# Kernel tuning notes

Measured on AMD Instinct MI355X. Metric: run time of the kernel, lower is better.

## Reference

```python
import jax, jax.numpy as jnp
import numpy as np

NUM_LAYER = 5
NUM_FEATURES = 128
DIM = 256
NUM_BOND_TYPE = 6
NUM_BOND_DIR = 3
BN_EPS = 1e-5


def setup_inputs() -> dict:
    key = jax.random.key(0)
    ks = jax.random.split(key, 16)
    N, E = 100000, 400000
    x = jax.random.normal(ks[0], (N, NUM_FEATURES), dtype=jnp.float32)
    edge_index = jax.random.randint(ks[1], (2, E), 0, N, dtype=jnp.int32)
    edge_attr = jax.random.randint(ks[2], (E, 2), 0, 3, dtype=jnp.int32)
    s = 0.05
    Wl = jax.random.normal(ks[3], (NUM_FEATURES, DIM), dtype=jnp.float32) * s
    bl = jnp.zeros((DIM,), dtype=jnp.float32)
    W1 = jax.random.normal(ks[4], (NUM_LAYER, DIM, 2 * DIM), dtype=jnp.float32) * s
    b1 = jnp.zeros((NUM_LAYER, 2 * DIM), dtype=jnp.float32)
    W2 = jax.random.normal(ks[5], (NUM_LAYER, 2 * DIM, DIM), dtype=jnp.float32) * s
    b2 = jnp.zeros((NUM_LAYER, DIM), dtype=jnp.float32)
    E1 = jax.random.normal(ks[6], (NUM_LAYER, NUM_BOND_TYPE, DIM), dtype=jnp.float32) * s
    E2 = jax.random.normal(ks[7], (NUM_LAYER, NUM_BOND_DIR, DIM), dtype=jnp.float32) * s
    gamma = jnp.ones((NUM_LAYER, DIM), dtype=jnp.float32)
    beta = jnp.zeros((NUM_LAYER, DIM), dtype=jnp.float32)
    return {"x": x, "edge_index": edge_index, "edge_attr": edge_attr,
            "Wl": Wl, "bl": bl, "W1": W1, "b1": b1, "W2": W2, "b2": b2,
            "E1": E1, "E2": E2, "gamma": gamma, "beta": beta}


def reference(x, edge_index, edge_attr, Wl, bl, W1, b1, W2, b2, E1, E2, gamma, beta):
    N = x.shape[0]
    src, dst = edge_index[0], edge_index[1]
    bt, bd = edge_attr[:, 0], edge_attr[:, 1]
    # input projection + activation
    h = jax.nn.relu(x @ Wl + bl)  # [N, D]
    for l in range(NUM_LAYER):
        # edge embeddings (real edges) + self-loop embedding (attr = [4, 0])
        eemb = E1[l][bt] + E2[l][bd]                      # [E, D]
        self_emb = E1[l][4] + E2[l][0]                    # [D]
        msg = h[src] + eemb                               # gather + add
        agg = jax.ops.segment_sum(msg, dst, num_segments=N)
        agg = agg + h + self_emb                          # self-loop messages
        # 2-layer MLP update
        hid = jax.nn.relu(agg @ W1[l] + b1[l])
        out = hid @ W2[l] + b2[l]
        # BatchNorm1d (training mode: batch stats, biased variance)
        mean = jnp.mean(out, axis=0)
        var = jnp.mean((out - mean) ** 2, axis=0)
        h = gamma[l] * (out - mean) * jax.lax.rsqrt(var + BN_EPS) + beta[l]
    # JK = 'last'
    return h
```

## Files before the change

### kernel.cpp

```cpp
#include <hip/hip_runtime.h>
#include <hip/hip_bf16.h>


typedef __bf16 bf16x8 __attribute__((ext_vector_type(8)));
typedef __bf16 bf16x4 __attribute__((ext_vector_type(4)));
typedef float f32x4 __attribute__((ext_vector_type(4)));

#define LDSTRIDE 40

__global__ __launch_bounds__(256, 2)
void gemm0_kernel(const float* __restrict__ Av, const __bf16* __restrict__ BT,
                  const float* __restrict__ bias, float* __restrict__ Cv,
                  int M, int K, int Nc)
{
    __shared__ __bf16 As[128 * LDSTRIDE];
    __shared__ __bf16 Bs[128 * LDSTRIDE];

    const int tid  = threadIdx.x;
    const int wave = tid >> 6;
    const int lane = tid & 63;
    const int quad = lane >> 4;
    const int l16  = lane & 15;
    const int wm   = wave >> 1;
    const int wn   = wave & 1;

    const int col0 = blockIdx.x * 128;
    const int row0 = blockIdx.y * 128;

    f32x4 acc[4][4];
#pragma unroll
    for (int mt = 0; mt < 4; ++mt)
#pragma unroll
        for (int nt = 0; nt < 4; ++nt) acc[mt][nt] = (f32x4){0.f, 0.f, 0.f, 0.f};

    const int srow = tid >> 1;
    const int scol = (tid & 1) * 16;
    const int a_row = row0 + srow;
    const bool a_ok = (a_row < M);
    const __bf16* Bp = BT + (size_t)(col0 + srow) * K + scol;

    for (int k0 = 0; k0 < K; k0 += 32) {
        bf16x8 a0, a1;
        const float* Ap = Av + (size_t)a_row * K + k0 + scol;
        f32x4 x0 = {0,0,0,0}, x1 = {0,0,0,0}, x2 = {0,0,0,0}, x3 = {0,0,0,0};
        if (a_ok) {
            x0 = *(const f32x4*)(Ap);
            x1 = *(const f32x4*)(Ap + 4);
            x2 = *(const f32x4*)(Ap + 8);
            x3 = *(const f32x4*)(Ap + 12);
        }
#pragma unroll
        for (int j = 0; j < 4; ++j) {
            a0[j] = (__bf16)x0[j]; a0[4 + j] = (__bf16)x1[j];
            a1[j] = (__bf16)x2[j]; a1[4 + j] = (__bf16)x3[j];
        }
        bf16x8 b0 = *(const bf16x8*)(Bp + k0);
        bf16x8 b1 = *(const bf16x8*)(Bp + k0 + 8);

        __syncthreads();
        *(bf16x8*)&As[srow * LDSTRIDE + scol]     = a0;
        *(bf16x8*)&As[srow * LDSTRIDE + scol + 8] = a1;
        *(bf16x8*)&Bs[srow * LDSTRIDE + scol]     = b0;
        *(bf16x8*)&Bs[srow * LDSTRIDE + scol + 8] = b1;
        __syncthreads();

        bf16x8 af[4], bfr[4];
#pragma unroll
        for (int mt = 0; mt < 4; ++mt)
            af[mt] = *(const bf16x8*)&As[(wm * 64 + mt * 16 + l16) * LDSTRIDE + quad * 8];
#pragma unroll
        for (int nt = 0; nt < 4; ++nt)
            bfr[nt] = *(const bf16x8*)&Bs[(wn * 64 + nt * 16 + l16) * LDSTRIDE + quad * 8];

#pragma unroll
        for (int mt = 0; mt < 4; ++mt)
#pragma unroll
            for (int nt = 0; nt < 4; ++nt)
                acc[mt][nt] = __builtin_amdgcn_mfma_f32_16x16x32_bf16(
                    af[mt], bfr[nt], acc[mt][nt], 0, 0, 0);
    }

#pragma unroll
    for (int nt = 0; nt < 4; ++nt) {
        const int col = col0 + wn * 64 + nt * 16 + l16;
        const float b = bias[col];
#pragma unroll
        for (int mt = 0; mt < 4; ++mt) {
#pragma unroll
            for (int r = 0; r < 4; ++r) {
                const int row = row0 + wm * 64 + mt * 16 + quad * 4 + r;
                if (row < M) {
                    float v = fmaxf(acc[mt][nt][r] + b, 0.f);
                    Cv[(size_t)row * Nc + col] = v;
                }
            }
        }
    }
}

#define HST 136

__global__ __launch_bounds__(256, 3)
void fused_mlp_kernel(const __bf16* __restrict__ aggb,
                      const __bf16* __restrict__ W1T, const float* __restrict__ b1,
                      const __bf16* __restrict__ W2T, const float* __restrict__ b2,
                      float* __restrict__ out, float* __restrict__ sums, int M)
{
    __shared__ __bf16 As[64 * 256];
    __shared__ __bf16 hidS[64 * HST];

    const int tid  = threadIdx.x;
    const int wave = tid >> 6;
    const int lane = tid & 63;
    const int quad = lane >> 4;
    const int l16  = lane & 15;
    const int row0 = blockIdx.x * 64;

    {
        const int srow = tid >> 2;
        const int gb8  = (tid & 3) * 8;
        const int m = row0 + srow;
        bf16x8 v[8];
        if (m < M) {
            const __bf16* Ap = aggb + (size_t)m * 256 + gb8 * 8;
#pragma unroll
            for (int j = 0; j < 8; ++j) v[j] = *(const bf16x8*)(Ap + j * 8);
        } else {
#pragma unroll
            for (int j = 0; j < 8; ++j)
#pragma unroll
                for (int q = 0; q < 8; ++q) v[j][q] = (__bf16)0.f;
        }
#pragma unroll
        for (int j = 0; j < 8; ++j) {
            const int sg = (gb8 + j) ^ (srow & 7);
            *(bf16x8*)&As[srow * 256 + sg * 8] = v[j];
        }
    }
    __syncthreads();

    const int cb = wave * 64;
    f32x4 acc2[4][4];
#pragma unroll
    for (int mt = 0; mt < 4; ++mt)
#pragma unroll
        for (int nt = 0; nt < 4; ++nt) acc2[mt][nt] = (f32x4){0.f, 0.f, 0.f, 0.f};

#pragma unroll 1
    for (int c = 0; c < 4; ++c) {
        const int nbase = c * 128 + wave * 32;
        f32x4 acc1[4][2];
#pragma unroll
        for (int mt = 0; mt < 4; ++mt)
#pragma unroll
            for (int nt = 0; nt < 2; ++nt) acc1[mt][nt] = (f32x4){0.f, 0.f, 0.f, 0.f};

#pragma unroll
        for (int kk = 0; kk < 8; ++kk) {
            bf16x8 Bf[2];
#pragma unroll
            for (int nt = 0; nt < 2; ++nt)
                Bf[nt] = *(const bf16x8*)(W1T + (size_t)(nbase + nt * 16 + l16) * 256
                                          + kk * 32 + quad * 8);
            const int sg = (kk * 4 + quad) ^ (l16 & 7);
            bf16x8 af[4];
#pragma unroll
            for (int mt = 0; mt < 4; ++mt)
                af[mt] = *(const bf16x8*)&As[(mt * 16 + l16) * 256 + sg * 8];
#pragma unroll
            for (int mt = 0; mt < 4; ++mt)
#pragma unroll
                for (int nt = 0; nt < 2; ++nt)
                    acc1[mt][nt] = __builtin_amdgcn_mfma_f32_16x16x32_bf16(
                        af[mt], Bf[nt], acc1[mt][nt], 0, 0, 0);
        }

        __syncthreads();

#pragma unroll
        for (int nt = 0; nt < 2; ++nt) {
            const int lcol = wave * 32 + nt * 16 + l16;
            const float bb = b1[c * 128 + lcol];
#pragma unroll
            for (int mt = 0; mt < 4; ++mt)
#pragma unroll
                for (int r = 0; r < 4; ++r) {
                    float v = fmaxf(acc1[mt][nt][r] + bb, 0.f);
                    hidS[(mt * 16 + quad * 4 + r) * HST + lcol] = (__bf16)v;
                }
        }
        __syncthreads();

#pragma unroll
        for (int kk = 0; kk < 4; ++kk) {
            bf16x8 Hf[4], Bf2[4];
#pragma unroll
            for (int mt = 0; mt < 4; ++mt)
                Hf[mt] = *(const bf16x8*)&hidS[(mt * 16 + l16) * HST + kk * 32 + quad * 8];
#pragma unroll
            for (int nt = 0; nt < 4; ++nt)
                Bf2[nt] = *(const bf16x8*)(W2T + (size_t)(cb + nt * 16 + l16) * 512
                                           + c * 128 + kk * 32 + quad * 8);
#pragma unroll
            for (int mt = 0; mt < 4; ++mt)
#pragma unroll
                for (int nt = 0; nt < 4; ++nt)
                    acc2[mt][nt] = __builtin_amdgcn_mfma_f32_16x16x32_bf16(
                        Hf[mt], Bf2[nt], acc2[mt][nt], 0, 0, 0);
        }
    }

#pragma unroll
    for (int nt = 0; nt < 4; ++nt) {
        const int col = cb + nt * 16 + l16;
        const float bb = b2[col];
        float s = 0.f, ss = 0.f;
#pragma unroll
        for (int mt = 0; mt < 4; ++mt) {
#pragma unroll
            for (int r = 0; r < 4; ++r) {
                const int row = row0 + mt * 16 + quad * 4 + r;
                if (row < M) {
                    float v = acc2[mt][nt][r] + bb;
                    out[(size_t)row * 256 + col] = v;
                    s += v; ss += v * v;
                }
            }
        }
        s += __shfl_xor(s, 16); ss += __shfl_xor(ss, 16);
        s += __shfl_xor(s, 32); ss += __shfl_xor(ss, 32);
        if (lane < 16) {
            atomicAdd(&sums[col], s);
            atomicAdd(&sums[256 + col], ss);
        }
    }
}

__global__ void convert_wt_kernel(const float* __restrict__ W, __bf16* __restrict__ WT,
                                  int K, int Nc, int total)
{
    int i = blockIdx.x * 256 + threadIdx.x;
    if (i >= total) return;
    int kn = K * Nc;
    int l = i / kn;
    int rem = i - l * kn;
    int n = rem / K;
    int k = rem - n * K;
    WT[i] = (__bf16)W[(size_t)l * kn + (size_t)k * Nc + n];
}


__global__ void zero_counts_kernel(int* __restrict__ counts, int N)
{
    int i = blockIdx.x * 256 + threadIdx.x;
    if (i < N) counts[i] = 0;
}

__global__ void hist_kernel(const int* __restrict__ ei, int* __restrict__ counts, int E)
{
    int e = blockIdx.x * 256 + threadIdx.x;
    if (e < E) atomicAdd(&counts[ei[E + e]], 1);
}

__global__ void scan1_kernel(const int* __restrict__ counts, int* __restrict__ partial,
                             int* __restrict__ blocksums, int N)
{
    __shared__ int sm[256];
    int i = blockIdx.x * 256 + threadIdx.x;
    int v = (i < N) ? counts[i] : 0;
    sm[threadIdx.x] = v;
    __syncthreads();
    for (int off = 1; off < 256; off <<= 1) {
        int t = 0;
        if ((int)threadIdx.x >= off) t = sm[threadIdx.x - off];
        __syncthreads();
        if ((int)threadIdx.x >= off) sm[threadIdx.x] += t;
        __syncthreads();
    }
    if (i < N) partial[i] = sm[threadIdx.x] - v;
    if (threadIdx.x == 255) blocksums[blockIdx.x] = sm[255];
}

__global__ void scan2_kernel(int* __restrict__ blocksums, int NB)
{
    __shared__ int sm[1024];
    int v = ((int)threadIdx.x < NB) ? blocksums[threadIdx.x] : 0;
    sm[threadIdx.x] = v;
    __syncthreads();
    for (int off = 1; off < 1024; off <<= 1) {
        int t = 0;
        if ((int)threadIdx.x >= off) t = sm[threadIdx.x - off];
        __syncthreads();
        if ((int)threadIdx.x >= off) sm[threadIdx.x] += t;
        __syncthreads();
    }
    if ((int)threadIdx.x < NB) blocksums[threadIdx.x] = sm[threadIdx.x] - v;
}

__global__ void scan3_kernel(const int* __restrict__ partial, const int* __restrict__ blocksums,
                             int* __restrict__ rowptr, int* __restrict__ woff, int N, int E)
{
    int i = blockIdx.x * 256 + threadIdx.x;
    if (i < N) {
        int v = partial[i] + blocksums[blockIdx.x];
        rowptr[i] = v;
        woff[i] = v;
    }
    if (i == 0) rowptr[N] = E;
}

__global__ void scatter_sort_kernel(const int* __restrict__ ei, const int* __restrict__ ea,
                                    int* __restrict__ woff, int* __restrict__ sorted, int E)
{
    int e = blockIdx.x * 256 + threadIdx.x;
    if (e >= E) return;
    int dst = ei[E + e];
    int src = ei[e];
    int c = ea[2 * e] * 3 + ea[2 * e + 1];
    int pos = atomicAdd(&woff[dst], 1);
    sorted[pos] = (src << 4) | c;
}


__global__ void build_table_kernel(const float* __restrict__ E1, const float* __restrict__ E2,
                                   int l, float* __restrict__ tab, float* __restrict__ selfemb,
                                   float* __restrict__ sums)
{
    int b = blockIdx.x;
    int t = threadIdx.x;
    const float* e1 = E1 + (size_t)l * 6 * 256;
    const float* e2 = E2 + (size_t)l * 3 * 256;
    if (b < 9) {
        tab[b * 256 + t] = e1[(b / 3) * 256 + t] + e2[(b % 3) * 256 + t];
    } else {
        selfemb[t] = e1[4 * 256 + t] + e2[0 * 256 + t];
        sums[t] = 0.f;
        sums[256 + t] = 0.f;
    }
}

template<int APPLY_BN>
__global__ __launch_bounds__(256)
void gather_kernel(const float* __restrict__ out, const int* __restrict__ rowptr,
                   const int* __restrict__ sorted, const float* __restrict__ tab,
                   const float* __restrict__ selfemb, const float* __restrict__ scsh,
                   __bf16* __restrict__ aggb, int N)
{
    int n = blockIdx.x * 4 + (threadIdx.x >> 6);
    if (n >= N) return;
    int lane = threadIdx.x & 63;
    int f = lane * 4;

    f32x4 sc, sh;
    if (APPLY_BN) {
        sc = *(const f32x4*)(scsh + f);
        sh = *(const f32x4*)(scsh + 256 + f);
    }

    int r0 = rowptr[n];
    int r1 = rowptr[n + 1];

    f32x4 hv = *(const f32x4*)(out + (size_t)n * 256 + f);
    if (APPLY_BN) hv = hv * sc + sh;
    f32x4 acc = hv + *(const f32x4*)(selfemb + f);

    for (int e = r0; e < r1; ++e) {
        int v = sorted[e];
        f32x4 xv = *(const f32x4*)(out + (size_t)(v >> 4) * 256 + f);
        if (APPLY_BN) xv = xv * sc + sh;
        acc += xv + *(const f32x4*)(tab + (v & 15) * 256 + f);
    }
    bf16x4 o;
#pragma unroll
    for (int j = 0; j < 4; ++j) o[j] = (__bf16)acc[j];
    *(bf16x4*)(aggb + (size_t)n * 256 + f) = o;
}

__global__ void bn_finalize_kernel(const float* __restrict__ sums,
                                   const float* __restrict__ gamma,
                                   const float* __restrict__ beta,
                                   int l, int M, float* __restrict__ scsh)
{
    int c = threadIdx.x;
    float inv = 1.f / (float)M;
    float mean = sums[c] * inv;
    float var = sums[256 + c] * inv - mean * mean;
    float sc = gamma[l * 256 + c] * rsqrtf(var + 1e-5f);
    scsh[c] = sc;
    scsh[256 + c] = beta[l * 256 + c] - mean * sc;
}

__global__ __launch_bounds__(256)
void bn_apply_kernel(const float* __restrict__ out, const float* __restrict__ scsh,
                     float* __restrict__ h, int total4)
{
    int i = blockIdx.x * 256 + threadIdx.x;
    if (i >= total4) return;
    int cg = i & 63;
    f32x4 sc = ((const f32x4*)scsh)[cg];
    f32x4 sh = ((const f32x4*)scsh)[64 + cg];
    f32x4 v = ((const f32x4*)out)[i];
    ((f32x4*)h)[i] = v * sc + sh;
}

extern "C" void kernel_launch(void* const* d_in, const int* in_sizes, int n_in,
                              void* d_out, int out_size, void* d_ws, size_t ws_size,
                              hipStream_t stream)
{
    const float* x     = (const float*)d_in[0];
    const int*   ei    = (const int*)d_in[1];
    const int*   ea    = (const int*)d_in[2];
    const float* Wl    = (const float*)d_in[3];
    const float* bl    = (const float*)d_in[4];
    const float* W1    = (const float*)d_in[5];
    const float* b1    = (const float*)d_in[6];
    const float* W2    = (const float*)d_in[7];
    const float* b2    = (const float*)d_in[8];
    const float* E1    = (const float*)d_in[9];
    const float* E2    = (const float*)d_in[10];
    const float* gamma = (const float*)d_in[11];
    const float* beta  = (const float*)d_in[12];

    const int N = in_sizes[0] / 128;
    const int E = in_sizes[1] / 2;

    __bf16* aggb = (__bf16*)d_out;
    float*  hfin = (float*)d_out;

    float*  out  = (float*)d_ws;
    __bf16* WlT  = (__bf16*)(out + (size_t)N * 256);
    __bf16* W1T  = WlT + 256 * 128;
    __bf16* W2T  = W1T + 5 * 512 * 256;
    float*  tab  = (float*)(W2T + 5 * 256 * 512);
    float*  selfemb = tab + 9 * 256;
    float*  sums = selfemb + 256;
    float*  scsh = sums + 512;
    int*    counts = (int*)(scsh + 512);
    int*    partial = counts + N;
    int*    rowptr  = partial + N;
    int*    woff    = rowptr + N + 1;
    int*    sorted  = woff + N;
    int*    blocksums = sorted + E;

    const int NB = (N + 255) / 256;
    const int EB = (E + 255) / 256;

    zero_counts_kernel<<<NB, 256, 0, stream>>>(counts, N);
    hist_kernel<<<EB, 256, 0, stream>>>(ei, counts, E);
    scan1_kernel<<<NB, 256, 0, stream>>>(counts, partial, blocksums, N);
    scan2_kernel<<<1, 1024, 0, stream>>>(blocksums, NB);
    scan3_kernel<<<NB, 256, 0, stream>>>(partial, blocksums, rowptr, woff, N, E);
    scatter_sort_kernel<<<EB, 256, 0, stream>>>(ei, ea, woff, sorted, E);

    convert_wt_kernel<<<(128 * 256 + 255) / 256, 256, 0, stream>>>(Wl, WlT, 128, 256, 128 * 256);
    convert_wt_kernel<<<(5 * 256 * 512 + 255) / 256, 256, 0, stream>>>(W1, W1T, 256, 512, 5 * 256 * 512);
    convert_wt_kernel<<<(5 * 512 * 256 + 255) / 256, 256, 0, stream>>>(W2, W2T, 512, 256, 5 * 512 * 256);

    const int mtiles128 = (N + 127) / 128;
    const int mtiles64  = (N + 63) / 64;
    const int total4 = N * 64;
    const int ew_blocks = (total4 + 255) / 256;
    const int gb = (N + 3) / 4;

    gemm0_kernel<<<dim3(2, mtiles128), 256, 0, stream>>>(x, WlT, bl, out, N, 128, 256);

    for (int l = 0; l < 5; ++l) {
        build_table_kernel<<<10, 256, 0, stream>>>(E1, E2, l, tab, selfemb, sums);
        if (l == 0)
            gather_kernel<0><<<gb, 256, 0, stream>>>(out, rowptr, sorted, tab, selfemb,
                                                     scsh, aggb, N);
        else
            gather_kernel<1><<<gb, 256, 0, stream>>>(out, rowptr, sorted, tab, selfemb,
                                                     scsh, aggb, N);
        fused_mlp_kernel<<<mtiles64, 256, 0, stream>>>(
            aggb, W1T + (size_t)l * 512 * 256, b1 + l * 512,
            W2T + (size_t)l * 256 * 512, b2 + l * 256, out, sums, N);
        bn_finalize_kernel<<<1, 256, 0, stream>>>(sums, gamma, beta, l, N, scsh);
    }
    bn_apply_kernel<<<ew_blocks, 256, 0, stream>>>(out, scsh, hfin, total4);
}
```

Before: 1.494 ms.

## Software-pipeline fused MLP with double-buffered hidden tile and replicated BN sums

The fused MLP kernel now processes the hidden dimension in 8 chunks of 64 rather than 4 of 128. Hidden activations go into a double-buffered LDS tile, so the first GEMM for chunk c overlaps the second GEMM for chunk c-1 with one barrier per iteration instead of two. W1 fragments are preloaded into registers at the top of each iteration. BatchNorm sum atomics are spread over 8 replicas keyed by block index to reduce atomic contention, and the finalize kernel reduces them. This costs more loop iterations and more register pressure.

```diff
diff --git a/kernel.cpp b/kernel.cpp
--- a/kernel.cpp
+++ b/kernel.cpp
@@ -98,7 +98,7 @@
     }
 }
 
-#define HST 136
+#define HST 72
 
 __global__ __launch_bounds__(256, 3)
 void fused_mlp_kernel(const __bf16* __restrict__ aggb,
@@ -107,7 +107,7 @@
                       float* __restrict__ out, float* __restrict__ sums, int M)
 {
     __shared__ __bf16 As[64 * 256];
-    __shared__ __bf16 hidS[64 * HST];
+    __shared__ __bf16 hidS[2][64 * HST];
 
     const int tid  = threadIdx.x;
     const int wave = tid >> 6;
@@ -137,7 +137,6 @@
             *(bf16x8*)&As[srow * 256 + sg * 8] = v[j];
         }
     }
-    __syncthreads();
 
     const int cb = wave * 64;
     f32x4 acc2[4][4];
@@ -146,70 +145,75 @@
 #pragma unroll
         for (int nt = 0; nt < 4; ++nt) acc2[mt][nt] = (f32x4){0.f, 0.f, 0.f, 0.f};
 
+    const __bf16* W1p = W1T + (size_t)(wave * 16 + l16) * 256 + quad * 8;
+    const __bf16* W2p = W2T + (size_t)(cb + l16) * 512 + quad * 8;
+
 #pragma unroll 1
-    for (int c = 0; c < 4; ++c) {
-        const int nbase = c * 128 + wave * 32;
-        f32x4 acc1[4][2];
-#pragma unroll
-        for (int mt = 0; mt < 4; ++mt)
-#pragma unroll
-            for (int nt = 0; nt < 2; ++nt) acc1[mt][nt] = (f32x4){0.f, 0.f, 0.f, 0.f};
-
-#pragma unroll
-        for (int kk = 0; kk < 8; ++kk) {
-            bf16x8 Bf[2];
-#pragma unroll
-            for (int nt = 0; nt < 2; ++nt)
-                Bf[nt] = *(const bf16x8*)(W1T + (size_t)(nbase + nt * 16 + l16) * 256
-                                          + kk * 32 + quad * 8);
-            const int sg = (kk * 4 + quad) ^ (l16 & 7);
-            bf16x8 af[4];
+    for (int c = 0; c <= 8; ++c) {
+        __syncthreads();
+
+        bf16x8 W1f[8];
+        if (c < 8) {
+            const __bf16* p = W1p + (size_t)(c * 64) * 256;
+#pragma unroll
+            for (int kk = 0; kk < 8; ++kk)
+                W1f[kk] = *(const bf16x8*)(p + kk * 32);
+        }
+
+        if (c >= 1) {
+            bf16x8 W2f[4][2];
+#pragma unroll
+            for (int nt = 0; nt < 4; ++nt)
+#pragma unroll
+                for (int kkl = 0; kkl < 2; ++kkl)
+                    W2f[nt][kkl] = *(const bf16x8*)(W2p + (size_t)(nt * 16) * 512
+                                                    + (c - 1) * 64 + kkl * 32);
+            const __bf16* buf = hidS[(c - 1) & 1];
+#pragma unroll
+            for (int kkl = 0; kkl < 2; ++kkl) {
+                bf16x8 Hf[4];
+#pragma unroll
+                for (int mt = 0; mt < 4; ++mt)
+                    Hf[mt] = *(const bf16x8*)&buf[(mt * 16 + l16) * HST + kkl * 32 + quad * 8];
+#pragma unroll
+                for (int mt = 0; mt < 4; ++mt)
+#pragma unroll
+                    for (int nt = 0; nt < 4; ++nt)
+                        acc2[mt][nt] = __builtin_amdgcn_mfma_f32_16x16x32_bf16(
+                            Hf[mt], W2f[nt][kkl], acc2[mt][nt], 0, 0, 0);
+            }
+        }
+
+        if (c < 8) {
+            f32x4 acc1[4];
+#pragma unroll
+            for (int mt = 0; mt < 4; ++mt) acc1[mt] = (f32x4){0.f, 0.f, 0.f, 0.f};
+#pragma unroll
+            for (int kk = 0; kk < 8; ++kk) {
+                const int sg = (kk * 4 + quad) ^ (l16 & 7);
+                bf16x8 af[4];
+#pragma unroll
+                for (int mt = 0; mt < 4; ++mt)
+                    af[mt] = *(const bf16x8*)&As[(mt * 16 + l16) * 256 + sg * 8];
+#pragma unroll
+                for (int mt = 0; mt < 4; ++mt)
+                    acc1[mt] = __builtin_amdgcn_mfma_f32_16x16x32_bf16(
+                        af[mt], W1f[kk], acc1[mt], 0, 0, 0);
+            }
+            __bf16* buf = hidS[c & 1];
+            const int lcol = wave * 16 + l16;
+            const float bb = b1[c * 64 + lcol];
 #pragma unroll
             for (int mt = 0; mt < 4; ++mt)
-                af[mt] = *(const bf16x8*)&As[(mt * 16 + l16) * 256 + sg * 8];
-#pragma unroll
-            for (int mt = 0; mt < 4; ++mt)
-#pragma unroll
-                for (int nt = 0; nt < 2; ++nt)
-                    acc1[mt][nt] = __builtin_amdgcn_mfma_f32_16x16x32_bf16(
-                        af[mt], Bf[nt], acc1[mt][nt], 0, 0, 0);
-        }
-
-        __syncthreads();
-
-#pragma unroll
-        for (int nt = 0; nt < 2; ++nt) {
-            const int lcol = wave * 32 + nt * 16 + l16;
-            const float bb = b1[c * 128 + lcol];
-#pragma unroll
-            for (int mt = 0; mt < 4; ++mt)
 #pragma unroll
                 for (int r = 0; r < 4; ++r) {
-                    float v = fmaxf(acc1[mt][nt][r] + bb, 0.f);
-                    hidS[(mt * 16 + quad * 4 + r) * HST + lcol] = (__bf16)v;
+                    float v = fmaxf(acc1[mt][r] + bb, 0.f);
+                    buf[(mt * 16 + quad * 4 + r) * HST + lcol] = (__bf16)v;
                 }
         }
-        __syncthreads();
-
-#pragma unroll
-        for (int kk = 0; kk < 4; ++kk) {
-            bf16x8 Hf[4], Bf2[4];
-#pragma unroll
-            for (int mt = 0; mt < 4; ++mt)
-                Hf[mt] = *(const bf16x8*)&hidS[(mt * 16 + l16) * HST + kk * 32 + quad * 8];
-#pragma unroll
-            for (int nt = 0; nt < 4; ++nt)
-                Bf2[nt] = *(const bf16x8*)(W2T + (size_t)(cb + nt * 16 + l16) * 512
-                                           + c * 128 + kk * 32 + quad * 8);
-#pragma unroll
-            for (int mt = 0; mt < 4; ++mt)
-#pragma unroll
-                for (int nt = 0; nt < 4; ++nt)
-                    acc2[mt][nt] = __builtin_amdgcn_mfma_f32_16x16x32_bf16(
-                        Hf[mt], Bf2[nt], acc2[mt][nt], 0, 0, 0);
-        }
-    }
-
+    }
+
+    float* srep = sums + (blockIdx.x & 7) * 512;
 #pragma unroll
     for (int nt = 0; nt < 4; ++nt) {
         const int col = cb + nt * 16 + l16;
@@ -230,8 +234,8 @@
         s += __shfl_xor(s, 16); ss += __shfl_xor(ss, 16);
         s += __shfl_xor(s, 32); ss += __shfl_xor(ss, 32);
         if (lane < 16) {
-            atomicAdd(&sums[col], s);
-            atomicAdd(&sums[256 + col], ss);
+            atomicAdd(&srep[col], s);
+            atomicAdd(&srep[256 + col], ss);
         }
     }
 }
@@ -334,8 +338,8 @@
         tab[b * 256 + t] = e1[(b / 3) * 256 + t] + e2[(b % 3) * 256 + t];
     } else {
         selfemb[t] = e1[4 * 256 + t] + e2[0 * 256 + t];
-        sums[t] = 0.f;
-        sums[256 + t] = 0.f;
+#pragma unroll
+        for (int r = 0; r < 16; ++r) sums[r * 256 + t] = 0.f;
     }
 }
 
@@ -382,9 +386,15 @@
                                    int l, int M, float* __restrict__ scsh)
 {
     int c = threadIdx.x;
+    float s = 0.f, ss = 0.f;
+#pragma unroll
+    for (int r = 0; r < 8; ++r) {
+        s  += sums[r * 512 + c];
+        ss += sums[r * 512 + 256 + c];
+    }
     float inv = 1.f / (float)M;
-    float mean = sums[c] * inv;
-    float var = sums[256 + c] * inv - mean * mean;
+    float mean = s * inv;
+    float var = ss * inv - mean * mean;
     float sc = gamma[l * 256 + c] * rsqrtf(var + 1e-5f);
     scsh[c] = sc;
     scsh[256 + c] = beta[l * 256 + c] - mean * sc;
@@ -434,7 +444,7 @@
     float*  tab  = (float*)(W2T + 5 * 256 * 512);
     float*  selfemb = tab + 9 * 256;
     float*  sums = selfemb + 256;
-    float*  scsh = sums + 512;
+    float*  scsh = sums + 4096;
     int*    counts = (int*)(scsh + 512);
     int*    partial = counts + N;
     int*    rowptr  = partial + N;
```

After: 1.461 ms. 1.02x faster.
